# Kernel optimization log

Measured on AMD Instinct MI355X. Metric: run time of the kernel, lower is better.

Reference implementation:

```python
import jax, jax.numpy as jnp
import numpy as np

B, C, S, HID = 64, 512, 28, 256  # batch, channels, spatial size, LSTM hidden


def _param(k, shape):
    return jax.random.normal(k, shape, jnp.float32) * 0.05


def setup_inputs() -> dict:
    key = jax.random.key(0)
    ks = jax.random.split(key, 19)
    inp = {"x": jax.random.normal(ks[0], (B, C, S, S), jnp.float32)}
    # vertical bidirectional LSTM (input C, hidden HID), torch gate order i,f,g,o
    inp["v_wih_f"] = _param(ks[1], (4 * HID, C))
    inp["v_whh_f"] = _param(ks[2], (4 * HID, HID))
    inp["v_b_f"] = _param(ks[3], (4 * HID,))
    inp["v_wih_b"] = _param(ks[4], (4 * HID, C))
    inp["v_whh_b"] = _param(ks[5], (4 * HID, HID))
    inp["v_b_b"] = _param(ks[6], (4 * HID,))
    # horizontal bidirectional LSTM (input 2*HID=512, hidden HID)
    inp["h_wih_f"] = _param(ks[7], (4 * HID, 2 * HID))
    inp["h_whh_f"] = _param(ks[8], (4 * HID, HID))
    inp["h_b_f"] = _param(ks[9], (4 * HID,))
    inp["h_wih_b"] = _param(ks[10], (4 * HID, 2 * HID))
    inp["h_whh_b"] = _param(ks[11], (4 * HID, HID))
    inp["h_b_b"] = _param(ks[12], (4 * HID,))
    # 1x1 conv 512 -> 100 (10x10 attention kernel logits)
    inp["conv_w"] = _param(ks[13], (100, 2 * HID))
    inp["conv_b"] = _param(ks[14], (100,))
    return inp


def _lstm_scan(xs, wih, whh, b):
    # xs: [T, N, D] -> h sequence [T, N, HID]
    hdim = whh.shape[1]
    def step(carry, xt):
        h, c = carry
        gates = xt @ wih.T + h @ whh.T + b  # [N, 4H]
        i, f, g, o = jnp.split(gates, 4, axis=-1)
        c = jax.nn.sigmoid(f) * c + jax.nn.sigmoid(i) * jnp.tanh(g)
        h = jax.nn.sigmoid(o) * jnp.tanh(c)
        return (h, c), h
    n = xs.shape[1]
    z = jnp.zeros((n, hdim), xs.dtype)
    _, hs = jax.lax.scan(step, (z, z), xs)
    return hs


def _bilstm(x, wf, uf, bf, wb, ub, bb):
    # x: [N, T, D] -> [N, T, 2*HID]
    xs = jnp.swapaxes(x, 0, 1)
    hf = _lstm_scan(xs, wf, uf, bf)
    hb = _lstm_scan(xs[::-1], wb, ub, bb)[::-1]
    return jnp.swapaxes(jnp.concatenate([hf, hb], axis=-1), 0, 1)


def reference(x, v_wih_f, v_whh_f, v_b_f, v_wih_b, v_whh_b, v_b_b,
              h_wih_f, h_whh_f, h_b_f, h_wih_b, h_whh_b, h_b_b,
              conv_w, conv_b):
    b, c, s, _ = x.shape
    xt = jnp.transpose(x, (0, 3, 2, 1))            # [B, W, H, C]
    # vertical LSTM: seq over W, batched over (B, H)
    v_in = jnp.transpose(xt, (0, 2, 1, 3)).reshape(b * s, s, c)
    v_out = _bilstm(v_in, v_wih_f, v_whh_f, v_b_f, v_wih_b, v_whh_b, v_b_b)
    v_out = jnp.transpose(v_out.reshape(b, s, s, 2 * HID), (0, 2, 1, 3))  # [B, W, H, 512]
    # horizontal LSTM: seq over H, batched over (B, W)
    h_in = v_out.reshape(b * s, s, 2 * HID)
    h_out = _bilstm(h_in, h_wih_f, h_whh_f, h_b_f, h_wih_b, h_whh_b, h_b_b)
    feat = jnp.transpose(h_out.reshape(b, s, s, 2 * HID), (0, 3, 2, 1))  # [B, 512, H, W]
    # 1x1 conv -> [B, 100, H, W], softmax over 100 kernel entries
    kern = jnp.einsum('bfhw,of->bohw', feat, conv_w) + conv_b[None, :, None, None]
    kern = jax.nn.softmax(kern, axis=1)
    # faithful to torch: C-order reshape [B,100,H,W] -> (B*H*W, 100) kernels
    w = kern.reshape(b, s * s, 100)
    # grouped dilated conv3d == weighted sum over dilation-3 sampled 10x10 grid
    x_s = x[:, :, ::3, ::3].reshape(b, c, 100)     # [B, C, 100]
    out = jnp.einsum('bpk,bck->bpc', w, x_s)       # [B, H*W, C]
    return out.reshape(b, c, s, s)                 # faithful C-order reshape
```

## Files before the change

### kernel.cpp

```cpp
#include <hip/hip_runtime.h>
#include <hip/hip_bf16.h>
#include <stdint.h>

typedef __hip_bfloat16 bf16_t;
typedef __attribute__((ext_vector_type(8))) short short8;
typedef __attribute__((ext_vector_type(4))) float f32x4;
typedef __attribute__((ext_vector_type(4))) unsigned int u32x4;
typedef unsigned long long ull;

#define MFMA16(a, b, c) __builtin_amdgcn_mfma_f32_16x16x32_bf16(a, b, c, 0, 0, 0)

#define NROW 50176
#define NBATCH 1792

__device__ __forceinline__ void g2l16(const void* g, void* l) {
  __builtin_amdgcn_global_load_lds(
      (const __attribute__((address_space(1))) unsigned int*)g,
      (__attribute__((address_space(3))) unsigned int*)l, 16, 0, 0);
}
__device__ __forceinline__ float sigm(float x) { return 1.0f / (1.0f + __expf(-x)); }
__device__ __forceinline__ float tanh_(float x) { return 2.0f / (1.0f + __expf(-2.0f * x)) - 1.0f; }
__device__ __forceinline__ void stc(bf16_t* p, float v) { *p = __float2bfloat16(v); }
__device__ __forceinline__ void stc(float* p, float v) { *p = v; }
__device__ __forceinline__ float bf2f(unsigned short u) {
  return __uint_as_float((unsigned int)u << 16);
}

struct CvtArgs {
  const float* src[8];
  bf16_t* dst[8];
  int n[8];
};
__global__ void cvt_all(CvtArgs a) {
  int arr = blockIdx.y;
  int i = blockIdx.x * 256 + threadIdx.x;
  if (i < a.n[arr]) a.dst[arr][i] = __float2bfloat16(a.src[arr][i]);
}

__global__ void transpose_x(const float* __restrict__ x, bf16_t* __restrict__ Xin) {
  int c0 = blockIdx.x * 128, h = blockIdx.y, b = blockIdx.z;
  __shared__ __align__(16) short tile[128 * 29];
  const float* xb = x + ((size_t)b * 512 + c0) * 784 + h * 28;
  for (int e = threadIdx.x; e < 128 * 28; e += 256) {
    int cc = e / 28, w = e - cc * 28;
    tile[cc * 29 + w] = __bfloat16_as_short(__float2bfloat16(xb[(size_t)cc * 784 + w]));
  }
  __syncthreads();
  size_t orow0 = (size_t)(b * 28 + h) * 28;
  short* os = (short*)Xin;
  for (int e = threadIdx.x; e < 28 * 128; e += 256) {
    int w = e >> 7, cc = e & 127;
    int c = c0 + cc;
    os[(size_t)(c >> 5) * NROW * 32 + (orow0 + w) * 32 + (c & 31)] = tile[cc * 29 + w];
  }
}

__global__ void build_xs(const float* __restrict__ x, bf16_t* __restrict__ xs) {
  int c = blockIdx.x, b = blockIdx.y;
  int k = threadIdx.x;
  const float* xr = x + ((size_t)b * 512 + c) * 784;
  float v = 0.0f;
  if (k < 100) { int kh = k / 10, kw = k - kh * 10; v = xr[kh * 84 + kw * 3]; }
  xs[((size_t)b * 512 + c) * 128 + k] = __float2bfloat16(v);
}

__global__ void pad_conv(const float* __restrict__ cw, const float* __restrict__ cb,
                         bf16_t* __restrict__ cwp, float* __restrict__ cbp,
                         unsigned int* __restrict__ bar) {
  int r = blockIdx.x;
  if (r == 0)
    for (int i = threadIdx.x; i < 7168; i += 128) bar[i] = 0;
  for (int i = threadIdx.x; i < 512; i += 128)
    cwp[r * 512 + i] = __float2bfloat16((r < 100) ? cw[r * 512 + i] : 0.0f);
  if (r == 0) cbp[threadIdx.x] = (threadIdx.x < 100) ? cb[threadIdx.x] : 0.0f;
}

template <typename CT, bool CPERM>
__global__ __launch_bounds__(256) void gemm_bt(
    const bf16_t* __restrict__ A, const bf16_t* __restrict__ B0,
    const bf16_t* __restrict__ B1, const float* __restrict__ bias0,
    const float* __restrict__ bias1, CT* __restrict__ C, int M, int N, int K) {
  __shared__ __align__(16) short As[2][128 * 32];
  __shared__ __align__(16) short Bs[2][128 * 32];
  int tid = threadIdx.x;
  int nb = blockIdx.x;
  int bm0 = blockIdx.y * 128, bn0 = nb * 128;
  int lrow = tid >> 2, lseg = tid & 3;
  const char* Ag = (const char*)A + ((size_t)(bm0 + lrow) * 32 + lseg * 8) * 2;
  size_t Aadv = (size_t)M * 64;
  const float* biasp;
  const char *Bg1, *Bg2;
  int js = 0;
  if (CPERM) {
    int dir = nb >> 3;
    js = nb & 7;
    const bf16_t* Bsel = dir ? B1 : B0;
    biasp = dir ? bias1 : bias0;
    int br1 = (lrow >> 5) * 256 + js * 32 + (lrow & 31);
    int br2 = ((lrow + 64) >> 5) * 256 + js * 32 + (lrow & 31);
    Bg1 = (const char*)(Bsel + (size_t)br1 * K) + lseg * 16;
    Bg2 = (const char*)(Bsel + (size_t)br2 * K) + lseg * 16;
  } else {
    biasp = bias0 + bn0;
    Bg1 = (const char*)(B0 + (size_t)(bn0 + lrow) * K) + lseg * 16;
    Bg2 = Bg1 + (size_t)64 * K * 2;
  }
  int w = tid >> 6, l = tid & 63, lm = l & 15, lq = l >> 4;
  int wm = w & 1, wn = w >> 1;
  f32x4 acc[4][4] = {};
  for (int k0 = 0; k0 < K; k0 += 64) {
#pragma unroll
    for (int p = 0; p < 2; p++) {
      g2l16(Ag, (char*)As[p] + tid * 16);
      g2l16(Ag + 4096, (char*)As[p] + 4096 + tid * 16);
      g2l16(Bg1, (char*)Bs[p] + tid * 16);
      g2l16(Bg2, (char*)Bs[p] + 4096 + tid * 16);
      Ag += Aadv; Bg1 += 64; Bg2 += 64;
    }
    __syncthreads();
#pragma unroll
    for (int p = 0; p < 2; p++) {
      short8 afr[4], bfr[4];
#pragma unroll
      for (int i = 0; i < 4; i++) {
        afr[i] = *(const short8*)&As[p][(wm * 64 + i * 16 + lm) * 32 + lq * 8];
        bfr[i] = *(const short8*)&Bs[p][(wn * 64 + i * 16 + lm) * 32 + lq * 8];
      }
#pragma unroll
      for (int mi = 0; mi < 4; mi++)
#pragma unroll
        for (int ni = 0; ni < 4; ni++) acc[mi][ni] = MFMA16(afr[mi], bfr[ni], acc[mi][ni]);
    }
    __syncthreads();
  }
  float bv[4];
#pragma unroll
  for (int ni = 0; ni < 4; ni++) {
    int cb = wn * 64 + ni * 16 + lm;
    bv[ni] = CPERM ? biasp[(cb >> 5) * 256 + js * 32 + (cb & 31)] : biasp[cb];
  }
#pragma unroll
  for (int mi = 0; mi < 4; mi++)
#pragma unroll
    for (int ni = 0; ni < 4; ni++) {
      int col = bn0 + wn * 64 + ni * 16 + lm;
#pragma unroll
      for (int r = 0; r < 4; r++) {
        size_t row = bm0 + wm * 64 + mi * 16 + lq * 4 + r;
        stc(&C[row * N + col], acc[mi][ni][r] + bv[ni]);
      }
    }
}

__global__ __launch_bounds__(256, 2) void lstm_scan(
    const bf16_t* __restrict__ G, const bf16_t* __restrict__ whh_f,
    const bf16_t* __restrict__ whh_b, bf16_t* __restrict__ hA,
    bf16_t* __restrict__ hB, bf16_t* __restrict__ outb,
    unsigned int* __restrict__ bar) {
  int dir = blockIdx.y;
  int js = blockIdx.x & 7;
  int rg = blockIdx.x >> 3;
  int tid = threadIdx.x, w = tid >> 6, l = tid & 63, lm = l & 15, lq = l >> 4;
  const short* whh = (const short*)(dir ? whh_b : whh_f);
  __shared__ __align__(16) short Ws[128 * 256];
  __shared__ __align__(16) short ht[64 * 40];
#pragma unroll
  for (int i = 0; i < 16; i++) {
    int segid = i * 256 + tid;
    int row = segid >> 5, seg = segid & 31;
    int gate = row >> 5, jj = row & 31;
    short8 v = *(const short8*)&whh[((size_t)(gate * 256 + js * 32 + jj)) * 256 + seg * 8];
    *(short8*)&Ws[row * 256 + ((seg ^ (row & 7)) * 8)] = v;
  }
  __syncthreads();
  unsigned int* cnt = bar + (((dir * 28 + rg) << 2) + w) * 16;
  int r0 = rg * 64 + w * 16;
  size_t dbase = (size_t)dir * 458752;
  const unsigned short* Gb = (const unsigned short*)G + (size_t)dir * 1024 + js * 128;
  float creg[2][4] = {};
  unsigned short gvs[2][4][4];
  auto load_gvs = [&](int tt) {
#pragma unroll
    for (int nj = 0; nj < 2; nj++)
#pragma unroll
      for (int r = 0; r < 4; r++) {
        int bi = r0 + lq * 4 + r;
        const unsigned short* gp = Gb + ((size_t)bi * 28 + tt) * 2048 + nj * 16 + lm;
#pragma unroll
        for (int gate = 0; gate < 4; gate++) gvs[nj][gate][r] = gp[gate * 32];
      }
  };
  load_gvs(dir ? 27 : 0);
  int srow = w * 16 + (l >> 2), sseg = l & 3;
  int sbi = rg * 64 + srow;
  int sbb = sbi / 28, srr = sbi - sbb * 28;
#pragma unroll 1
  for (int s = 0; s < 28; s++) {
    int t = dir ? 27 - s : s;
    f32x4 acc[4][2] = {};
    if (s > 0) {
      unsigned int tgt = 8u * (unsigned)s;
      while (__hip_atomic_load(cnt, __ATOMIC_RELAXED, __HIP_MEMORY_SCOPE_AGENT) < tgt)
        __builtin_amdgcn_s_sleep(1);
      const ull* hrp = (const ull*)((s & 1) ? hA : hB);
      ull hq[8][2];
#pragma unroll
      for (int kk = 0; kk < 8; kk++) {
        size_t off = dbase + (size_t)kk * 57344 + (size_t)(r0 + lm) * 32 + lq * 8;
        hq[kk][0] =
            __hip_atomic_load(hrp + (off >> 2), __ATOMIC_RELAXED, __HIP_MEMORY_SCOPE_AGENT);
        hq[kk][1] = __hip_atomic_load(hrp + (off >> 2) + 1, __ATOMIC_RELAXED,
                                      __HIP_MEMORY_SCOPE_AGENT);
      }
#pragma unroll
      for (int kk = 0; kk < 8; kk++) {
        short8 a;
        ((ull*)&a)[0] = hq[kk][0];
        ((ull*)&a)[1] = hq[kk][1];
        int bseg = ((kk * 4 + lq) ^ (lm & 7)) * 8;
#pragma unroll
        for (int gate = 0; gate < 4; gate++)
#pragma unroll
          for (int nj = 0; nj < 2; nj++) {
            short8 b = *(const short8*)&Ws[(gate * 32 + nj * 16 + lm) * 256 + bseg];
            acc[gate][nj] = MFMA16(a, b, acc[gate][nj]);
          }
      }
    }
#pragma unroll
    for (int nj = 0; nj < 2; nj++)
#pragma unroll
      for (int r = 0; r < 4; r++) {
        float gi = bf2f(gvs[nj][0][r]) + acc[0][nj][r];
        float gf = bf2f(gvs[nj][1][r]) + acc[1][nj][r];
        float gg = bf2f(gvs[nj][2][r]) + acc[2][nj][r];
        float go = bf2f(gvs[nj][3][r]) + acc[3][nj][r];
        float cn = sigm(gf) * creg[nj][r] + sigm(gi) * tanh_(gg);
        float hn = sigm(go) * tanh_(cn);
        creg[nj][r] = cn;
        ht[(w * 16 + lq * 4 + r) * 40 + nj * 16 + lm] =
            __bfloat16_as_short(__float2bfloat16(hn));
      }
    {
      u32x4 v = *(const u32x4*)&ht[srow * 40 + sseg * 8];
      ull* hwp = (ull*)((s & 1) ? hB : hA);
      size_t off = dbase + (size_t)js * 57344 + (size_t)sbi * 32 + sseg * 8;
      ull q0 = ((const ull*)&v)[0];
      ull q1 = ((const ull*)&v)[1];
      __hip_atomic_store(hwp + (off >> 2), q0, __ATOMIC_RELAXED, __HIP_MEMORY_SCOPE_AGENT);
      __hip_atomic_store(hwp + (off >> 2) + 1, q1, __ATOMIC_RELAXED,
                         __HIP_MEMORY_SCOPE_AGENT);
      short* ob = (short*)outb + (size_t)(dir * 8 + js) * NROW * 32;
      *(u32x4*)&ob[((size_t)sbb * 784 + (size_t)t * 28 + srr) * 32 + sseg * 8] = v;
    }
    if (s < 27) {
      asm volatile("s_waitcnt vmcnt(0)" ::: "memory");
      if (l == 0)
        __hip_atomic_fetch_add(cnt, 1u, __ATOMIC_RELAXED, __HIP_MEMORY_SCOPE_AGENT);
      load_gvs(dir ? 26 - s : s + 1);
    }
  }
}

__global__ __launch_bounds__(256) void softmax_scatter(const float* __restrict__ P,
                                                       bf16_t* __restrict__ Wscr) {
  int row = blockIdx.x * 4 + (threadIdx.x >> 6);
  int l = threadIdx.x & 63;
  int b = row / 784, q = row - b * 784;
  const float* pr = P + (size_t)row * 128;
  float v0 = (l < 100) ? pr[l] : -1e30f;
  float v1 = (l + 64 < 100) ? pr[l + 64] : -1e30f;
  float m = fmaxf(v0, v1);
  for (int off = 32; off > 0; off >>= 1) m = fmaxf(m, __shfl_down(m, off));
  m = __shfl(m, 0);
  float e0 = (l < 100) ? __expf(v0 - m) : 0.0f;
  float e1 = (l + 64 < 100) ? __expf(v1 - m) : 0.0f;
  float sum = e0 + e1;
  for (int off = 32; off > 0; off >>= 1) sum += __shfl_down(sum, off);
  sum = __shfl(sum, 0);
  float inv = 1.0f / sum;
  size_t base = (size_t)b * 784 * 128;
  if (l < 100) {
    int mm = l * 784 + q;
    Wscr[base + (size_t)(mm / 100) * 128 + (mm % 100)] = __float2bfloat16(e0 * inv);
  }
  int o = l + 64;
  if (o < 100) {
    int mm = o * 784 + q;
    Wscr[base + (size_t)(mm / 100) * 128 + (mm % 100)] = __float2bfloat16(e1 * inv);
  }
}

__global__ __launch_bounds__(256) void final_gemm(const bf16_t* __restrict__ Wscr,
                                                  const bf16_t* __restrict__ xs,
                                                  float* __restrict__ outp) {
  int m0 = blockIdx.x * 112, n0 = blockIdx.y * 128, b = blockIdx.z;
  int tid = threadIdx.x, w = tid >> 6, l = tid & 63, lm = l & 15, lq = l >> 4;
  const short* Ab = (const short*)Wscr + (size_t)b * 784 * 128;
  const short* Bb = (const short*)xs + (size_t)b * 512 * 128;
  f32x4 acc[7][2] = {};
#pragma unroll
  for (int kk = 0; kk < 4; kk++) {
    short8 b0 = *(const short8*)&Bb[(size_t)(n0 + w * 32 + lm) * 128 + kk * 32 + lq * 8];
    short8 b1 = *(const short8*)&Bb[(size_t)(n0 + w * 32 + 16 + lm) * 128 + kk * 32 + lq * 8];
#pragma unroll
    for (int mi = 0; mi < 7; mi++) {
      short8 a = *(const short8*)&Ab[(size_t)(m0 + mi * 16 + lm) * 128 + kk * 32 + lq * 8];
      acc[mi][0] = MFMA16(a, b0, acc[mi][0]);
      acc[mi][1] = MFMA16(a, b1, acc[mi][1]);
    }
  }
#pragma unroll
  for (int mi = 0; mi < 7; mi++)
#pragma unroll
    for (int ni = 0; ni < 2; ni++) {
      int c = n0 + w * 32 + ni * 16 + lm;
#pragma unroll
      for (int r = 0; r < 4; r++) {
        int p = m0 + mi * 16 + lq * 4 + r;
        outp[(size_t)b * 401408 + (size_t)p * 512 + c] = acc[mi][ni][r];
      }
    }
}

extern "C" void kernel_launch(void* const* d_in, const int* in_sizes, int n_in,
                              void* d_out, int out_size, void* d_ws, size_t ws_size,
                              hipStream_t stream) {
  const float* x = (const float*)d_in[0];
  const float* v_wih_f = (const float*)d_in[1];
  const float* v_whh_f = (const float*)d_in[2];
  const float* v_b_f = (const float*)d_in[3];
  const float* v_wih_b = (const float*)d_in[4];
  const float* v_whh_b = (const float*)d_in[5];
  const float* v_b_b = (const float*)d_in[6];
  const float* h_wih_f = (const float*)d_in[7];
  const float* h_whh_f = (const float*)d_in[8];
  const float* h_b_f = (const float*)d_in[9];
  const float* h_wih_b = (const float*)d_in[10];
  const float* h_whh_b = (const float*)d_in[11];
  const float* h_b_b = (const float*)d_in[12];
  const float* conv_w = (const float*)d_in[13];
  const float* conv_b = (const float*)d_in[14];

  char* ws = (char*)d_ws;
  bf16_t* Xin = (bf16_t*)(ws);
  bf16_t* Vout = (bf16_t*)(ws + 51380224);
  bf16_t* G = (bf16_t*)(ws + 102760448);
  float* P = (float*)(ws + 102760448);
  bf16_t* Wscr = (bf16_t*)(ws + 128450560);
  bf16_t* xs = (bf16_t*)(ws + 308281344);
  bf16_t* cwp = (bf16_t*)(ws + 316669952);
  float* cbp = (float*)(ws + 316801024);
  bf16_t* hstate = (bf16_t*)(ws + 316801536);
  unsigned int* bar = (unsigned int*)(ws + 318636544);
  bf16_t* wvf = (bf16_t*)(ws + 322306560);
  bf16_t* wvb = (bf16_t*)(ws + 323355136);
  bf16_t* uvf = (bf16_t*)(ws + 324403712);
  bf16_t* uvb = (bf16_t*)(ws + 324928000);
  bf16_t* whf = (bf16_t*)(ws + 325452288);
  bf16_t* whb = (bf16_t*)(ws + 326500864);
  bf16_t* uhf = (bf16_t*)(ws + 327549440);
  bf16_t* uhb = (bf16_t*)(ws + 328073728);
  bf16_t* Hout = Xin;

  CvtArgs ca;
  ca.src[0] = v_wih_f; ca.dst[0] = wvf; ca.n[0] = 524288;
  ca.src[1] = v_wih_b; ca.dst[1] = wvb; ca.n[1] = 524288;
  ca.src[2] = v_whh_f; ca.dst[2] = uvf; ca.n[2] = 262144;
  ca.src[3] = v_whh_b; ca.dst[3] = uvb; ca.n[3] = 262144;
  ca.src[4] = h_wih_f; ca.dst[4] = whf; ca.n[4] = 524288;
  ca.src[5] = h_wih_b; ca.dst[5] = whb; ca.n[5] = 524288;
  ca.src[6] = h_whh_f; ca.dst[6] = uhf; ca.n[6] = 262144;
  ca.src[7] = h_whh_b; ca.dst[7] = uhb; ca.n[7] = 262144;
  cvt_all<<<dim3(2048, 8), 256, 0, stream>>>(ca);

  transpose_x<<<dim3(4, 28, 64), 256, 0, stream>>>(x, Xin);
  build_xs<<<dim3(512, 64), 128, 0, stream>>>(x, xs);
  pad_conv<<<dim3(128), 128, 0, stream>>>(conv_w, conv_b, cwp, cbp, bar);

  gemm_bt<bf16_t, true><<<dim3(16, 392), 256, 0, stream>>>(
      Xin, wvf, wvb, v_b_f, v_b_b, G, NROW, 2048, 512);
  lstm_scan<<<dim3(224, 2), 256, 0, stream>>>(G, uvf, uvb, hstate, Xin, Vout, bar);

  gemm_bt<bf16_t, true><<<dim3(16, 392), 256, 0, stream>>>(
      Vout, whf, whb, h_b_f, h_b_b, G, NROW, 2048, 512);
  lstm_scan<<<dim3(224, 2), 256, 0, stream>>>(G, uhf, uhb, hstate, Vout, Hout, bar + 3584);

  gemm_bt<float, false><<<dim3(1, 392), 256, 0, stream>>>(
      Hout, cwp, cwp, cbp, cbp, P, NROW, 128, 512);
  softmax_scatter<<<dim3(12544), 256, 0, stream>>>(P, Wscr);
  final_gemm<<<dim3(7, 4, 64), 256, 0, stream>>>(Wscr, xs, (float*)d_out);
}
```

Before: 994.8 us.

## Stage bf16 GEMM epilogue through LDS for coalesced stores; fuse xs build into transpose

For the bf16 output GEMMs, the epilogue now writes the accumulator tile into shared memory, padded to a 130-element row stride, in two 64-row halves. It then writes each row to global memory with 16-byte vector stores instead of scattered 2-byte stores. The separate build_xs kernel is removed, and the dilation-3 subsampled x plus its zero padding are written from the transpose_x tile already in LDS. This costs extra syncthreads and LDS traffic in the epilogue but should improve global write coalescing for the large gate matrices.

```diff
diff --git a/kernel.cpp b/kernel.cpp
--- a/kernel.cpp
+++ b/kernel.cpp
@@ -37,7 +37,8 @@
   if (i < a.n[arr]) a.dst[arr][i] = __float2bfloat16(a.src[arr][i]);
 }
 
-__global__ void transpose_x(const float* __restrict__ x, bf16_t* __restrict__ Xin) {
+__global__ void transpose_x(const float* __restrict__ x, bf16_t* __restrict__ Xin,
+                            bf16_t* __restrict__ xs) {
   int c0 = blockIdx.x * 128, h = blockIdx.y, b = blockIdx.z;
   __shared__ __align__(16) short tile[128 * 29];
   const float* xb = x + ((size_t)b * 512 + c0) * 784 + h * 28;
@@ -53,15 +54,20 @@
     int c = c0 + cc;
     os[(size_t)(c >> 5) * NROW * 32 + (orow0 + w) * 32 + (c & 31)] = tile[cc * 29 + w];
   }
-}
-
-__global__ void build_xs(const float* __restrict__ x, bf16_t* __restrict__ xs) {
-  int c = blockIdx.x, b = blockIdx.y;
-  int k = threadIdx.x;
-  const float* xr = x + ((size_t)b * 512 + c) * 784;
-  float v = 0.0f;
-  if (k < 100) { int kh = k / 10, kw = k - kh * 10; v = xr[kh * 84 + kw * 3]; }
-  xs[((size_t)b * 512 + c) * 128 + k] = __float2bfloat16(v);
+  short* xss = (short*)xs;
+  if (h % 3 == 0) {
+    int kh = h / 3;
+    for (int e = threadIdx.x; e < 1280; e += 256) {
+      int cc = e / 10, kw = e - cc * 10;
+      xss[((size_t)(b * 512) + c0 + cc) * 128 + kh * 10 + kw] = tile[cc * 29 + 3 * kw];
+    }
+  }
+  if (h == 0) {
+    for (int e = threadIdx.x; e < 128 * 28; e += 256) {
+      int cc = e / 28, kp = e - cc * 28;
+      xss[((size_t)(b * 512) + c0 + cc) * 128 + 100 + kp] = 0;
+    }
+  }
 }
 
 __global__ void pad_conv(const float* __restrict__ cw, const float* __restrict__ cb,
@@ -80,8 +86,9 @@
     const bf16_t* __restrict__ A, const bf16_t* __restrict__ B0,
     const bf16_t* __restrict__ B1, const float* __restrict__ bias0,
     const float* __restrict__ bias1, CT* __restrict__ C, int M, int N, int K) {
-  __shared__ __align__(16) short As[2][128 * 32];
-  __shared__ __align__(16) short Bs[2][128 * 32];
+  __shared__ __align__(16) short smem[16384];
+  short(*As)[4096] = (short(*)[4096])smem;
+  short(*Bs)[4096] = (short(*)[4096])(smem + 8192);
   int tid = threadIdx.x;
   int nb = blockIdx.x;
   int bm0 = blockIdx.y * 128, bn0 = nb * 128;
@@ -139,17 +146,45 @@
     int cb = wn * 64 + ni * 16 + lm;
     bv[ni] = CPERM ? biasp[(cb >> 5) * 256 + js * 32 + (cb & 31)] : biasp[cb];
   }
-#pragma unroll
-  for (int mi = 0; mi < 4; mi++)
-#pragma unroll
-    for (int ni = 0; ni < 4; ni++) {
-      int col = bn0 + wn * 64 + ni * 16 + lm;
-#pragma unroll
-      for (int r = 0; r < 4; r++) {
-        size_t row = bm0 + wm * 64 + mi * 16 + lq * 4 + r;
-        stc(&C[row * N + col], acc[mi][ni][r] + bv[ni]);
-      }
-    }
+  if constexpr (sizeof(CT) == 2) {
+#pragma unroll 1
+    for (int mh = 0; mh < 2; mh++) {
+      if (wm == mh) {
+#pragma unroll
+        for (int mi = 0; mi < 4; mi++)
+#pragma unroll
+          for (int ni = 0; ni < 4; ni++)
+#pragma unroll
+            for (int r = 0; r < 4; r++) {
+              int row = mi * 16 + lq * 4 + r;
+              int col = wn * 64 + ni * 16 + lm;
+              smem[row * 130 + col] =
+                  __bfloat16_as_short(__float2bfloat16(acc[mi][ni][r] + bv[ni]));
+            }
+      }
+      __syncthreads();
+      {
+        int row = tid >> 2, seg = tid & 3;
+        short* Crow = (short*)C + (size_t)(bm0 + mh * 64 + row) * N + bn0 + seg * 32;
+#pragma unroll
+        for (int j = 0; j < 4; j++)
+          *(u32x4*)(Crow + j * 8) = *(const u32x4*)&smem[row * 130 + seg * 32 + j * 8];
+      }
+      __syncthreads();
+    }
+  } else {
+#pragma unroll
+    for (int mi = 0; mi < 4; mi++)
+#pragma unroll
+      for (int ni = 0; ni < 4; ni++) {
+        int col = bn0 + wn * 64 + ni * 16 + lm;
+#pragma unroll
+        for (int r = 0; r < 4; r++) {
+          size_t row = bm0 + wm * 64 + mi * 16 + lq * 4 + r;
+          stc(&C[row * N + col], acc[mi][ni][r] + bv[ni]);
+        }
+      }
+  }
 }
 
 __global__ __launch_bounds__(256, 2) void lstm_scan(
@@ -374,8 +409,7 @@
   ca.src[7] = h_whh_b; ca.dst[7] = uhb; ca.n[7] = 262144;
   cvt_all<<<dim3(2048, 8), 256, 0, stream>>>(ca);
 
-  transpose_x<<<dim3(4, 28, 64), 256, 0, stream>>>(x, Xin);
-  build_xs<<<dim3(512, 64), 128, 0, stream>>>(x, xs);
+  transpose_x<<<dim3(4, 28, 64), 256, 0, stream>>>(x, Xin, xs);
   pad_conv<<<dim3(128), 128, 0, stream>>>(conv_w, conv_b, cwp, cbp, bar);
 
   gemm_bt<bf16_t, true><<<dim3(16, 392), 256, 0, stream>>>(
```

After: 1.007 ms. About the same (+1.2%).
